# Performance work log

Hardware: AMD Instinct MI355X
Metric: run time of the kernel (lower is better)

Reference implementation:

```python
import jax, jax.numpy as jnp
import numpy as np

B, S, D, E, K = 2, 2048, 512, 8, 2
H = 4 * D  # 2048


def setup_inputs() -> dict:
    key = jax.random.key(0)
    ks = jax.random.split(key, 6)
    x = jax.random.normal(ks[0], (B, S, D), dtype=jnp.float32)
    # parameters, matching torch init (randn weights, zero biases)
    w1 = jax.random.normal(ks[1], (E, D, H), dtype=jnp.float32)
    w2 = jax.random.normal(ks[2], (E, H, D), dtype=jnp.float32)
    b1 = jnp.zeros((E, H), dtype=jnp.float32)
    b2 = jnp.zeros((E, D), dtype=jnp.float32)
    # nn.Linear(D, E): kaiming-uniform-ish; plain uniform is fine for a baseline
    lim = 1.0 / np.sqrt(D)
    router_w = jax.random.uniform(ks[3], (D, E), dtype=jnp.float32, minval=-lim, maxval=lim)
    router_b = jax.random.uniform(ks[4], (E,), dtype=jnp.float32, minval=-lim, maxval=lim)
    return {"x": x, "w1": w1, "w2": w2, "b1": b1, "b2": b2,
            "router_w": router_w, "router_b": router_b}


def reference(x, w1, w2, b1, b2, router_w, router_b):
    # router: [b,s,e]
    router_logits = jnp.einsum('bsd,de->bse', x, router_w) + router_b
    top_k_logits, top_k_indices = jax.lax.top_k(router_logits, K)   # [b,s,k]
    top_k_probs = jax.nn.softmax(top_k_logits, axis=-1)             # [b,s,k]
    masks = jax.nn.one_hot(top_k_indices, E, dtype=x.dtype)          # [b,s,k,e]
    # dense all-expert MLP (faithful to source: every expert on every token)
    h = jnp.einsum('bsd,edh->bseh', x, w1) + b1                      # [b,s,e,4d]
    h = jax.nn.gelu(h, approximate=False)                            # exact gelu
    y = jnp.einsum('bseh,ehd->bsed', h, w2) + b2                     # [b,s,e,d]
    # combine: mask each expert output by routed prob and sum over top-k
    out = jnp.einsum('bsed,bske,bsk->bsd', y, masks, top_k_probs)    # [b,s,d]
    return out
```

## Files before the change

kernel.cpp:

```cpp
#include <hip/hip_runtime.h>
#include <math.h>

typedef unsigned short u16;
typedef __bf16 bf16x8 __attribute__((ext_vector_type(8)));
typedef float f32x4 __attribute__((ext_vector_type(4)));

#define T_TOKENS 4096
#define D_DIM    512
#define H_DIM    2048
#define E_NUM    8
#define CAP      4096
#define NSLOT    (T_TOKENS * 2)
#define NCHUNK   16

__device__ __forceinline__ u16 f2bf(float f) {
  unsigned int u = __builtin_bit_cast(unsigned int, f);
  u = (u + 0x7fffu + ((u >> 16) & 1u)) >> 16;
  return (u16)u;
}

__device__ __forceinline__ void gload16(const void* g, void* l) {
  __builtin_amdgcn_global_load_lds(
      (__attribute__((address_space(1))) void*)(g),
      (__attribute__((address_space(3))) void*)(l), 16, 0, 0);
}

__device__ __forceinline__ float gelu_fast(float v) {
  float u = v * __fmaf_rn(0.071354817f, v * v, 1.59576912f);
  float e = __expf(-u);
  return v * __builtin_amdgcn_rcpf(1.0f + e);
}

__global__ __launch_bounds__(256) void transpose_both_kernel(const float* __restrict__ w1,
                                                             const float* __restrict__ w2,
                                                             u16* __restrict__ w1t,
                                                             u16* __restrict__ w2t) {
  __shared__ float tile[64][67];
  int bid = blockIdx.x;
  const float* in; u16* out; int R, C;
  if (bid < 2048) { in = w1; out = w1t; R = D_DIM; C = H_DIM; }
  else            { bid -= 2048; in = w2; out = w2t; R = H_DIM; C = D_DIM; }
  const int e = bid >> 8;
  const int t = bid & 255;
  const int nCx = C >> 6;
  const int c0 = (t % nCx) * 64, r0 = (t / nCx) * 64;
  const float* src = in + (size_t)e * D_DIM * H_DIM;
  u16* dst = out + (size_t)e * D_DIM * H_DIM;
  const int tid = threadIdx.x;
  {
    const int row = tid >> 2, cc = (tid & 3) * 16;
    const float* s = src + (size_t)(r0 + row) * C + c0 + cc;
#pragma unroll
    for (int j = 0; j < 4; j++)
      *(float4*)(&tile[row][cc + 4 * j]) = *(const float4*)(s + 4 * j);
  }
  __syncthreads();
  {
    const int c = tid >> 2, rc = (tid & 3) * 16;
    u16 buf[16];
#pragma unroll
    for (int j = 0; j < 16; j++) buf[j] = f2bf(tile[rc + j][c]);
    u16* d = dst + (size_t)(c0 + c) * R + r0 + rc;
    *(uint4*)(d)     = *(uint4*)(&buf[0]);
    *(uint4*)(d + 8) = *(uint4*)(&buf[8]);
  }
}

__global__ __launch_bounds__(256) void router_kernel(const float* __restrict__ x,
                                                     const float* __restrict__ rw,
                                                     const float* __restrict__ rb,
                                                     int* __restrict__ topk_idx,
                                                     float* __restrict__ topk_p,
                                                     u16* __restrict__ xb,
                                                     float* __restrict__ outz) {
  {
    float4 z = {0.f, 0.f, 0.f, 0.f};
    float4* o = (float4*)(outz + (size_t)blockIdx.x * 2048);
    o[threadIdx.x] = z;
    o[threadIdx.x + 256] = z;
  }
  const int lane = threadIdx.x & 63;
  const int t = blockIdx.x * 4 + (threadIdx.x >> 6);
  const float* xr = x + (size_t)t * D_DIM + lane * 8;
  float xv[8];
  *(float4*)(&xv[0]) = *(const float4*)(xr);
  *(float4*)(&xv[4]) = *(const float4*)(xr + 4);
  ushort4 o0, o1;
  o0.x = f2bf(xv[0]); o0.y = f2bf(xv[1]); o0.z = f2bf(xv[2]); o0.w = f2bf(xv[3]);
  o1.x = f2bf(xv[4]); o1.y = f2bf(xv[5]); o1.z = f2bf(xv[6]); o1.w = f2bf(xv[7]);
  ushort4* xo = (ushort4*)(xb + (size_t)t * D_DIM + lane * 8);
  xo[0] = o0; xo[1] = o1;

  float acc[8] = {0.f,0.f,0.f,0.f,0.f,0.f,0.f,0.f};
#pragma unroll
  for (int j = 0; j < 8; j++) {
    const float4* w = (const float4*)(rw + (size_t)(lane * 8 + j) * E_NUM);
    float4 w0 = w[0], w1 = w[1];
    acc[0] += xv[j] * w0.x; acc[1] += xv[j] * w0.y;
    acc[2] += xv[j] * w0.z; acc[3] += xv[j] * w0.w;
    acc[4] += xv[j] * w1.x; acc[5] += xv[j] * w1.y;
    acc[6] += xv[j] * w1.z; acc[7] += xv[j] * w1.w;
  }
#pragma unroll
  for (int off = 32; off > 0; off >>= 1) {
#pragma unroll
    for (int e = 0; e < 8; e++) acc[e] += __shfl_down(acc[e], off);
  }
  if (lane == 0) {
    float l[8];
#pragma unroll
    for (int e = 0; e < 8; e++) l[e] = acc[e] + rb[e];
    int i0 = 0; float v0 = l[0];
#pragma unroll
    for (int e = 1; e < 8; e++) if (l[e] > v0) { v0 = l[e]; i0 = e; }
    int i1 = -1; float v1 = -3.4e38f;
#pragma unroll
    for (int e = 0; e < 8; e++) if (e != i0 && l[e] > v1) { v1 = l[e]; i1 = e; }
    float p1 = expf(v1 - v0);
    float s = 1.0f + p1;
    topk_idx[t * 2] = i0; topk_idx[t * 2 + 1] = i1;
    topk_p[t * 2] = 1.0f / s; topk_p[t * 2 + 1] = p1 / s;
  }
}

__global__ __launch_bounds__(256) void count_kernel(const int* __restrict__ topk_idx,
                                                    int* __restrict__ chunkcnt) {
  const int b = blockIdx.x, tid = threadIdx.x, lane = tid & 63, w = tid >> 6;
  const int t = b * 256 + tid;
  const int i0 = topk_idx[t * 2], i1 = topk_idx[t * 2 + 1];
  __shared__ int ws[4][E_NUM];
#pragma unroll
  for (int e = 0; e < E_NUM; e++) {
    unsigned long long m = __ballot(i0 == e || i1 == e);
    if (lane == 0) ws[w][e] = (int)__popcll(m);
  }
  __syncthreads();
  if (tid < E_NUM)
    chunkcnt[b * E_NUM + tid] = ws[0][tid] + ws[1][tid] + ws[2][tid] + ws[3][tid];
}

__global__ __launch_bounds__(256) void scatter_kernel(const int* __restrict__ topk_idx,
                                                      const float* __restrict__ topk_p,
                                                      const int* __restrict__ chunkcnt,
                                                      int* __restrict__ slot_list,
                                                      float* __restrict__ prob_list,
                                                      int* __restrict__ counts) {
  const int e = blockIdx.x & 7, chunk = blockIdx.x >> 3;
  const int tid = threadIdx.x, lane = tid & 63, w = tid >> 6;
  int base = 0;
  for (int c = 0; c < chunk; ++c) base += chunkcnt[c * E_NUM + e];
  const int t = chunk * 256 + tid;
  const int i0 = topk_idx[t * 2], i1 = topk_idx[t * 2 + 1];
  int flag = 0, slot = 0; float p = 0.f;
  if (i0 == e)      { flag = 1; slot = t * 2;     p = topk_p[t * 2]; }
  else if (i1 == e) { flag = 1; slot = t * 2 + 1; p = topk_p[t * 2 + 1]; }
  unsigned long long m = __ballot(flag);
  __shared__ int wsum[4];
  if (lane == 0) wsum[w] = (int)__popcll(m);
  const int wpre = (int)__popcll(m & ((1ull << lane) - 1ull));
  __syncthreads();
  int wb = base;
#pragma unroll
  for (int j = 0; j < 4; j++) if (j < w) wb += wsum[j];
  if (flag) { slot_list[e * CAP + wb + wpre] = slot; prob_list[e * CAP + wb + wpre] = p; }
  if (chunk == NCHUNK - 1 && tid == 0)
    counts[e] = base + wsum[0] + wsum[1] + wsum[2] + wsum[3];
}

__global__ __launch_bounds__(256, 2) void gemm1_kernel(const u16* __restrict__ xb,
                                                       const u16* __restrict__ w1t,
                                                       const float* __restrict__ b1,
                                                       const int* __restrict__ slot_list,
                                                       const float* __restrict__ prob_list,
                                                       const int* __restrict__ counts,
                                                       u16* __restrict__ hbuf) {
  const int f = blockIdx.x;
  const int e  = f & 7;
  const int g  = f >> 3;
  const int cx = g & 15;
  const int rt = g >> 4;
  const int cnt = counts[e];
  const int rbase = rt * 64;
  if (rbase >= cnt) return;
  const int n0 = cx * 128;

  __shared__ __align__(16) u16 At[3][64 * 64];
  __shared__ __align__(16) u16 Bt[3][128 * 64];

  const int tid = threadIdx.x, lane = tid & 63, wid = tid >> 6;
  const int wr = wid >> 1, wc = wid & 1;
  const int lr8 = lane >> 3;
  const int sx = lane & 7;
  const int kperm = (sx ^ lr8) * 8;
  const int lrow = lane & 15, lk = lane >> 4;

  const u16* pa[2]; int loa[2];
#pragma unroll
  for (int i = 0; i < 2; i++) {
    const int row = (wid * 2 + i) * 8 + lr8;
    const int grow = rbase + row;
    int tok = 0;
    if (grow < cnt) tok = slot_list[e * CAP + grow] >> 1;
    pa[i] = xb + (size_t)tok * D_DIM + kperm;
    loa[i] = (wid * 2 + i) * 512;
  }
  const u16* pb[4]; int lob[4];
#pragma unroll
  for (int i = 0; i < 4; i++) {
    const int row = (wid * 4 + i) * 8 + lr8;
    pb[i] = w1t + ((size_t)e * H_DIM + n0 + row) * D_DIM + kperm;
    lob[i] = (wid * 4 + i) * 512;
  }

  f32x4 acc[2][4];
#pragma unroll
  for (int i = 0; i < 2; i++)
#pragma unroll
    for (int j = 0; j < 4; j++) acc[i][j] = (f32x4){0.f, 0.f, 0.f, 0.f};

  auto stage = [&](int k0, int b) {
#pragma unroll
    for (int i = 0; i < 2; i++) gload16(pa[i] + k0, &At[b][loa[i]]);
#pragma unroll
    for (int i = 0; i < 4; i++) gload16(pb[i] + k0, &Bt[b][lob[i]]);
  };

  stage(0, 0); stage(64, 1); stage(128, 2);
  const int nt = D_DIM / 64;
  int cur = 0;
  for (int t = 0; t < nt; ++t) {
    if (t < nt - 2)       { asm volatile("s_waitcnt vmcnt(12)" ::: "memory"); }
    else if (t == nt - 2) { asm volatile("s_waitcnt vmcnt(6)" ::: "memory"); }
    else                  { asm volatile("s_waitcnt vmcnt(0)" ::: "memory"); }
    __builtin_amdgcn_sched_barrier(0);
    __builtin_amdgcn_s_barrier();
    bf16x8 afr[2][2], bfr[4][2];
#pragma unroll
    for (int ks = 0; ks < 2; ks++) {
#pragma unroll
      for (int fq = 0; fq < 2; fq++)
        afr[fq][ks] = *(const bf16x8*)(&At[cur][(wr * 32 + fq * 16 + lrow) * 64 + ((ks * 4 + lk) ^ sx) * 8]);
#pragma unroll
      for (int fq = 0; fq < 4; fq++)
        bfr[fq][ks] = *(const bf16x8*)(&Bt[cur][(wc * 64 + fq * 16 + lrow) * 64 + ((ks * 4 + lk) ^ sx) * 8]);
    }
    asm volatile("s_waitcnt lgkmcnt(0)" ::: "memory");
    __builtin_amdgcn_sched_barrier(0);
    __builtin_amdgcn_s_barrier();
    if (t + 3 < nt) stage((t + 3) * 64, cur);
    __builtin_amdgcn_sched_barrier(0);
    __builtin_amdgcn_s_setprio(1);
#pragma unroll
    for (int ks = 0; ks < 2; ks++)
#pragma unroll
      for (int fr = 0; fr < 2; fr++)
#pragma unroll
        for (int fc = 0; fc < 4; fc++)
          acc[fr][fc] = __builtin_amdgcn_mfma_f32_16x16x32_bf16(afr[fr][ks], bfr[fc][ks], acc[fr][fc], 0, 0, 0);
    __builtin_amdgcn_s_setprio(0);
    cur = (cur == 2) ? 0 : cur + 1;
  }

  float bias[4];
#pragma unroll
  for (int fc = 0; fc < 4; fc++) bias[fc] = b1[e * H_DIM + n0 + wc * 64 + fc * 16 + lrow];
#pragma unroll
  for (int fr = 0; fr < 2; fr++) {
#pragma unroll
    for (int reg = 0; reg < 4; reg++) {
      const int rloc = wr * 32 + fr * 16 + lk * 4 + reg;
      const int grow = rbase + rloc;
      if (grow < cnt) {
        const int slot = slot_list[e * CAP + grow];
        const float p  = prob_list[e * CAP + grow];
        u16* dst = hbuf + (size_t)slot * H_DIM + n0 + wc * 64 + lrow;
#pragma unroll
        for (int fc = 0; fc < 4; fc++) {
          float v = acc[fr][fc][reg] + bias[fc];
          dst[fc * 16] = f2bf(gelu_fast(v) * p);
        }
      }
    }
  }
}

__global__ __launch_bounds__(256, 2) void gemm2_kernel(const u16* __restrict__ hbuf,
                                                       const u16* __restrict__ w2t,
                                                       const float* __restrict__ b2,
                                                       const int* __restrict__ slot_list,
                                                       const float* __restrict__ prob_list,
                                                       const int* __restrict__ counts,
                                                       float* __restrict__ out) {
  const int f = blockIdx.x;
  const int e  = f & 7;
  const int g  = f >> 3;
  const int cx = g & 3;
  const int rt = g >> 2;
  const int cnt = counts[e];
  const int rbase = rt * 64;
  if (rbase >= cnt) return;
  const int n0 = cx * 128;

  __shared__ __align__(16) u16 At[3][64 * 64];
  __shared__ __align__(16) u16 Bt[3][128 * 64];

  const int tid = threadIdx.x, lane = tid & 63, wid = tid >> 6;
  const int wr = wid >> 1, wc = wid & 1;
  const int lr8 = lane >> 3;
  const int sx = lane & 7;
  const int kperm = (sx ^ lr8) * 8;
  const int lrow = lane & 15, lk = lane >> 4;

  const u16* pa[2]; int loa[2];
#pragma unroll
  for (int i = 0; i < 2; i++) {
    const int row = (wid * 2 + i) * 8 + lr8;
    const int grow = rbase + row;
    int slot = 0;
    if (grow < cnt) slot = slot_list[e * CAP + grow];
    pa[i] = hbuf + (size_t)slot * H_DIM + kperm;
    loa[i] = (wid * 2 + i) * 512;
  }
  const u16* pb[4]; int lob[4];
#pragma unroll
  for (int i = 0; i < 4; i++) {
    const int row = (wid * 4 + i) * 8 + lr8;
    pb[i] = w2t + ((size_t)e * D_DIM + n0 + row) * H_DIM + kperm;
    lob[i] = (wid * 4 + i) * 512;
  }

  f32x4 acc[2][4];
#pragma unroll
  for (int i = 0; i < 2; i++)
#pragma unroll
    for (int j = 0; j < 4; j++) acc[i][j] = (f32x4){0.f, 0.f, 0.f, 0.f};

  auto stage = [&](int k0, int b) {
#pragma unroll
    for (int i = 0; i < 2; i++) gload16(pa[i] + k0, &At[b][loa[i]]);
#pragma unroll
    for (int i = 0; i < 4; i++) gload16(pb[i] + k0, &Bt[b][lob[i]]);
  };

  stage(0, 0); stage(64, 1); stage(128, 2);
  const int nt = H_DIM / 64;
  int cur = 0;
  for (int t = 0; t < nt; ++t) {
    if (t < nt - 2)       { asm volatile("s_waitcnt vmcnt(12)" ::: "memory"); }
    else if (t == nt - 2) { asm volatile("s_waitcnt vmcnt(6)" ::: "memory"); }
    else                  { asm volatile("s_waitcnt vmcnt(0)" ::: "memory"); }
    __builtin_amdgcn_sched_barrier(0);
    __builtin_amdgcn_s_barrier();
    bf16x8 afr[2][2], bfr[4][2];
#pragma unroll
    for (int ks = 0; ks < 2; ks++) {
#pragma unroll
      for (int fq = 0; fq < 2; fq++)
        afr[fq][ks] = *(const bf16x8*)(&At[cur][(wr * 32 + fq * 16 + lrow) * 64 + ((ks * 4 + lk) ^ sx) * 8]);
#pragma unroll
      for (int fq = 0; fq < 4; fq++)
        bfr[fq][ks] = *(const bf16x8*)(&Bt[cur][(wc * 64 + fq * 16 + lrow) * 64 + ((ks * 4 + lk) ^ sx) * 8]);
    }
    asm volatile("s_waitcnt lgkmcnt(0)" ::: "memory");
    __builtin_amdgcn_sched_barrier(0);
    __builtin_amdgcn_s_barrier();
    if (t + 3 < nt) stage((t + 3) * 64, cur);
    __builtin_amdgcn_sched_barrier(0);
    __builtin_amdgcn_s_setprio(1);
#pragma unroll
    for (int ks = 0; ks < 2; ks++)
#pragma unroll
      for (int fr = 0; fr < 2; fr++)
#pragma unroll
        for (int fc = 0; fc < 4; fc++)
          acc[fr][fc] = __builtin_amdgcn_mfma_f32_16x16x32_bf16(afr[fr][ks], bfr[fc][ks], acc[fr][fc], 0, 0, 0);
    __builtin_amdgcn_s_setprio(0);
    cur = (cur == 2) ? 0 : cur + 1;
  }

#pragma unroll
  for (int fr = 0; fr < 2; fr++) {
#pragma unroll
    for (int reg = 0; reg < 4; reg++) {
      const int rloc = wr * 32 + fr * 16 + lk * 4 + reg;
      const int grow = rbase + rloc;
      if (grow < cnt) {
        const int slot = slot_list[e * CAP + grow];
        const float p  = prob_list[e * CAP + grow];
        float* dst = out + (size_t)(slot >> 1) * D_DIM + n0 + wc * 64 + lrow;
#pragma unroll
        for (int fc = 0; fc < 4; fc++) {
          float v = acc[fr][fc][reg] + p * b2[e * D_DIM + n0 + wc * 64 + fc * 16 + lrow];
          atomicAdd(&dst[fc * 16], v);
        }
      }
    }
  }
}

extern "C" void kernel_launch(void* const* d_in, const int* in_sizes, int n_in,
                              void* d_out, int out_size, void* d_ws, size_t ws_size,
                              hipStream_t stream) {
  const float* x  = (const float*)d_in[0];
  const float* w1 = (const float*)d_in[1];
  const float* w2 = (const float*)d_in[2];
  const float* b1 = (const float*)d_in[3];
  const float* b2 = (const float*)d_in[4];
  const float* rw = (const float*)d_in[5];
  const float* rb = (const float*)d_in[6];
  float* out = (float*)d_out;

  char* ws = (char*)d_ws;
  size_t off = 0;
  auto alloc = [&](size_t bytes) -> void* {
    void* p = ws + off;
    off = (off + bytes + 255) & ~(size_t)255;
    return p;
  };
  int*   counts    = (int*)alloc(E_NUM * 4);
  int*   chunkcnt  = (int*)alloc(NCHUNK * E_NUM * 4);
  int*   slot_list = (int*)alloc((size_t)E_NUM * CAP * 4);
  float* prob_list = (float*)alloc((size_t)E_NUM * CAP * 4);
  int*   topk_idx  = (int*)alloc((size_t)T_TOKENS * 2 * 4);
  float* topk_p    = (float*)alloc((size_t)T_TOKENS * 2 * 4);
  u16*   xb        = (u16*)alloc((size_t)T_TOKENS * D_DIM * 2);
  u16*   w1t       = (u16*)alloc((size_t)E_NUM * H_DIM * D_DIM * 2);
  u16*   w2t       = (u16*)alloc((size_t)E_NUM * H_DIM * D_DIM * 2);
  u16*   hbuf      = (u16*)alloc((size_t)NSLOT * H_DIM * 2);

  transpose_both_kernel<<<4096, 256, 0, stream>>>(w1, w2, w1t, w2t);
  router_kernel<<<T_TOKENS / 4, 256, 0, stream>>>(x, rw, rb, topk_idx, topk_p, xb, out);
  count_kernel<<<NCHUNK, 256, 0, stream>>>(topk_idx, chunkcnt);
  scatter_kernel<<<NCHUNK * E_NUM, 256, 0, stream>>>(topk_idx, topk_p, chunkcnt, slot_list, prob_list, counts);
  gemm1_kernel<<<E_NUM * 64 * 16, 256, 0, stream>>>(xb, w1t, b1, slot_list, prob_list, counts, hbuf);
  gemm2_kernel<<<E_NUM * 64 * 4, 256, 0, stream>>>(hbuf, w2t, b2, slot_list, prob_list, counts, out);
}
```

Measured before the change: 145.2 us.

## Switch grouped GEMMs to double-buffered LDS with one barrier, 2D grid, occupancy 3

Both expert GEMM kernels drop the three-stage LDS ring for a two-stage double buffer. The next tile is issued right after a single barrier per k-step, and the wait on loads is a full vmcnt(0). Less LDS per block lets launch bounds ask for three blocks per CU instead of two. The grid becomes 2D, with column tiles on x and expert/row tile on y, which changes block scheduling order and which weights and activations sit in cache together. The trade-off is a shallower prefetch depth that exposes more global-load latency per block, and the bet is that extra occupancy hides it.

```diff
diff --git a/kernel.cpp b/kernel.cpp
--- a/kernel.cpp
+++ b/kernel.cpp
@@ -167,25 +167,22 @@
     counts[e] = base + wsum[0] + wsum[1] + wsum[2] + wsum[3];
 }
 
-__global__ __launch_bounds__(256, 2) void gemm1_kernel(const u16* __restrict__ xb,
+__global__ __launch_bounds__(256, 3) void gemm1_kernel(const u16* __restrict__ xb,
                                                        const u16* __restrict__ w1t,
                                                        const float* __restrict__ b1,
                                                        const int* __restrict__ slot_list,
                                                        const float* __restrict__ prob_list,
                                                        const int* __restrict__ counts,
                                                        u16* __restrict__ hbuf) {
-  const int f = blockIdx.x;
-  const int e  = f & 7;
-  const int g  = f >> 3;
-  const int cx = g & 15;
-  const int rt = g >> 4;
+  const int e  = blockIdx.y >> 6;
+  const int rt = blockIdx.y & 63;
   const int cnt = counts[e];
   const int rbase = rt * 64;
   if (rbase >= cnt) return;
-  const int n0 = cx * 128;
-
-  __shared__ __align__(16) u16 At[3][64 * 64];
-  __shared__ __align__(16) u16 Bt[3][128 * 64];
+  const int n0 = blockIdx.x * 128;
+
+  __shared__ __align__(16) u16 At[2][64 * 64];
+  __shared__ __align__(16) u16 Bt[2][128 * 64];
 
   const int tid = threadIdx.x, lane = tid & 63, wid = tid >> 6;
   const int wr = wid >> 1, wc = wid & 1;
@@ -225,15 +222,14 @@
     for (int i = 0; i < 4; i++) gload16(pb[i] + k0, &Bt[b][lob[i]]);
   };
 
-  stage(0, 0); stage(64, 1); stage(128, 2);
+  stage(0, 0);
   const int nt = D_DIM / 64;
   int cur = 0;
   for (int t = 0; t < nt; ++t) {
-    if (t < nt - 2)       { asm volatile("s_waitcnt vmcnt(12)" ::: "memory"); }
-    else if (t == nt - 2) { asm volatile("s_waitcnt vmcnt(6)" ::: "memory"); }
-    else                  { asm volatile("s_waitcnt vmcnt(0)" ::: "memory"); }
+    asm volatile("s_waitcnt vmcnt(0)" ::: "memory");
     __builtin_amdgcn_sched_barrier(0);
     __builtin_amdgcn_s_barrier();
+    if (t + 1 < nt) stage((t + 1) * 64, cur ^ 1);
     bf16x8 afr[2][2], bfr[4][2];
 #pragma unroll
     for (int ks = 0; ks < 2; ks++) {
@@ -246,9 +242,6 @@
     }
     asm volatile("s_waitcnt lgkmcnt(0)" ::: "memory");
     __builtin_amdgcn_sched_barrier(0);
-    __builtin_amdgcn_s_barrier();
-    if (t + 3 < nt) stage((t + 3) * 64, cur);
-    __builtin_amdgcn_sched_barrier(0);
     __builtin_amdgcn_s_setprio(1);
 #pragma unroll
     for (int ks = 0; ks < 2; ks++)
@@ -258,7 +251,7 @@
         for (int fc = 0; fc < 4; fc++)
           acc[fr][fc] = __builtin_amdgcn_mfma_f32_16x16x32_bf16(afr[fr][ks], bfr[fc][ks], acc[fr][fc], 0, 0, 0);
     __builtin_amdgcn_s_setprio(0);
-    cur = (cur == 2) ? 0 : cur + 1;
+    cur ^= 1;
   }
 
   float bias[4];
@@ -284,25 +277,22 @@
   }
 }
 
-__global__ __launch_bounds__(256, 2) void gemm2_kernel(const u16* __restrict__ hbuf,
+__global__ __launch_bounds__(256, 3) void gemm2_kernel(const u16* __restrict__ hbuf,
                                                        const u16* __restrict__ w2t,
                                                        const float* __restrict__ b2,
                                                        const int* __restrict__ slot_list,
                                                        const float* __restrict__ prob_list,
                                                        const int* __restrict__ counts,
                                                        float* __restrict__ out) {
-  const int f = blockIdx.x;
-  const int e  = f & 7;
-  const int g  = f >> 3;
-  const int cx = g & 3;
-  const int rt = g >> 2;
+  const int e  = blockIdx.y >> 6;
+  const int rt = blockIdx.y & 63;
   const int cnt = counts[e];
   const int rbase = rt * 64;
   if (rbase >= cnt) return;
-  const int n0 = cx * 128;
-
-  __shared__ __align__(16) u16 At[3][64 * 64];
-  __shared__ __align__(16) u16 Bt[3][128 * 64];
+  const int n0 = blockIdx.x * 128;
+
+  __shared__ __align__(16) u16 At[2][64 * 64];
+  __shared__ __align__(16) u16 Bt[2][128 * 64];
 
   const int tid = threadIdx.x, lane = tid & 63, wid = tid >> 6;
   const int wr = wid >> 1, wc = wid & 1;
@@ -342,15 +332,14 @@
     for (int i = 0; i < 4; i++) gload16(pb[i] + k0, &Bt[b][lob[i]]);
   };
 
-  stage(0, 0); stage(64, 1); stage(128, 2);
+  stage(0, 0);
   const int nt = H_DIM / 64;
   int cur = 0;
   for (int t = 0; t < nt; ++t) {
-    if (t < nt - 2)       { asm volatile("s_waitcnt vmcnt(12)" ::: "memory"); }
-    else if (t == nt - 2) { asm volatile("s_waitcnt vmcnt(6)" ::: "memory"); }
-    else                  { asm volatile("s_waitcnt vmcnt(0)" ::: "memory"); }
+    asm volatile("s_waitcnt vmcnt(0)" ::: "memory");
     __builtin_amdgcn_sched_barrier(0);
     __builtin_amdgcn_s_barrier();
+    if (t + 1 < nt) stage((t + 1) * 64, cur ^ 1);
     bf16x8 afr[2][2], bfr[4][2];
 #pragma unroll
     for (int ks = 0; ks < 2; ks++) {
@@ -363,9 +352,6 @@
     }
     asm volatile("s_waitcnt lgkmcnt(0)" ::: "memory");
     __builtin_amdgcn_sched_barrier(0);
-    __builtin_amdgcn_s_barrier();
-    if (t + 3 < nt) stage((t + 3) * 64, cur);
-    __builtin_amdgcn_sched_barrier(0);
     __builtin_amdgcn_s_setprio(1);
 #pragma unroll
     for (int ks = 0; ks < 2; ks++)
@@ -375,7 +361,7 @@
         for (int fc = 0; fc < 4; fc++)
           acc[fr][fc] = __builtin_amdgcn_mfma_f32_16x16x32_bf16(afr[fr][ks], bfr[fc][ks], acc[fr][fc], 0, 0, 0);
     __builtin_amdgcn_s_setprio(0);
-    cur = (cur == 2) ? 0 : cur + 1;
+    cur ^= 1;
   }
 
 #pragma unroll
@@ -432,6 +418,6 @@
   router_kernel<<<T_TOKENS / 4, 256, 0, stream>>>(x, rw, rb, topk_idx, topk_p, xb, out);
   count_kernel<<<NCHUNK, 256, 0, stream>>>(topk_idx, chunkcnt);
   scatter_kernel<<<NCHUNK * E_NUM, 256, 0, stream>>>(topk_idx, topk_p, chunkcnt, slot_list, prob_list, counts);
-  gemm1_kernel<<<E_NUM * 64 * 16, 256, 0, stream>>>(xb, w1t, b1, slot_list, prob_list, counts, hbuf);
-  gemm2_kernel<<<E_NUM * 64 * 4, 256, 0, stream>>>(hbuf, w2t, b2, slot_list, prob_list, counts, out);
-}
+  gemm1_kernel<<<dim3(16, E_NUM * 64), 256, 0, stream>>>(xb, w1t, b1, slot_list, prob_list, counts, hbuf);
+  gemm2_kernel<<<dim3(4, E_NUM * 64), 256, 0, stream>>>(hbuf, w2t, b2, slot_list, prob_list, counts, out);
+}
```

Result: faster. 120.0 us (-17.3%).
